# Kernel optimization log

Measured on AMD Instinct MI355X. Metric: run time of the kernel, lower is better.

Reference implementation:

```python
import jax, jax.numpy as jnp
import numpy as np

STRIDES = (8, 16, 32)
H = W = 640
SCORE_T = 0.5
NMS_T = 0.4


def setup_inputs() -> dict:
    key = jax.random.key(0)
    ks = jax.random.split(key, 9)
    feats = [(H // s) * (W // s) for s in STRIDES]  # 6400, 1600, 400
    d = {}
    for i, n in enumerate(feats):
        d[f"score{i}"] = jax.random.normal(ks[i], (1, n, 1), jnp.float32)
        d[f"bbox{i}"] = jax.random.normal(ks[3 + i], (1, n, 4), jnp.float32)
        d[f"kps{i}"] = jax.random.normal(ks[6 + i], (1, n, 10), jnp.float32)
    return d


def _anchors(stride):
    fh, fw = H // stride, W // stride
    yv, xv = jnp.meshgrid(jnp.arange(fh), jnp.arange(fw), indexing="ij")
    return jnp.stack([xv, yv], -1).reshape(-1, 2).astype(jnp.float32) * stride


def _decode(score, bbox, kps, stride):
    pts = _anchors(stride)                      # [N,2]
    s = jax.nn.sigmoid(score[0]).reshape(-1)    # [N]
    d = bbox[0] * stride                        # [N,4]
    x1 = pts[:, 0] - d[:, 0]
    y1 = pts[:, 1] - d[:, 1]
    x2 = pts[:, 0] + d[:, 2]
    y2 = pts[:, 1] + d[:, 3]
    b = jnp.stack([x1, y1, x2, y2], -1)         # [N,4]
    kd = (kps[0] * stride).reshape(-1, 5, 2)    # [N,5,2] (px,py pairs)
    k = (pts[:, None, :] + kd).reshape(-1, 10)  # [N,10]
    return s, b, k


def _iou(b):
    area = (b[:, 2] - b[:, 0]) * (b[:, 3] - b[:, 1])
    lt = jnp.maximum(b[:, None, :2], b[None, :, :2])
    rb = jnp.minimum(b[:, None, 2:], b[None, :, 2:])
    wh = jnp.clip(rb - lt, 0.0)
    inter = wh[..., 0] * wh[..., 1]
    return inter / (area[:, None] + area[None, :] - inter + 1e-9)


def _nms_keep(iou, valid, thresh):
    # greedy NMS on score-sorted boxes: keep i iff no earlier kept j has IoU>thresh
    n = valid.shape[0]
    def body(keep, xs):
        i, row = xs
        suppressed = jnp.any(keep & (row > thresh))
        keep = keep.at[i].set(valid[i] & ~suppressed)
        return keep, None
    keep, _ = jax.lax.scan(body, jnp.zeros(n, bool), (jnp.arange(n), iou))
    return keep


def reference(score0, score1, score2, bbox0, bbox1, bbox2, kps0, kps1, kps2):
    parts = [
        _decode(s, b, k, st)
        for s, b, k, st in zip(
            (score0, score1, score2), (bbox0, bbox1, bbox2), (kps0, kps1, kps2), STRIDES
        )
    ]
    scores = jnp.concatenate([p[0] for p in parts])  # [8400]
    boxes = jnp.concatenate([p[1] for p in parts])   # [8400,4]
    kpss = jnp.concatenate([p[2] for p in parts])    # [8400,10]
    order = jnp.argsort(-scores)                     # score-descending (NMS order)
    scores = scores[order]
    boxes = boxes[order]
    kpss = kpss[order]
    valid = scores > SCORE_T                         # threshold mask
    iou = _iou(jax.lax.stop_gradient(boxes))         # [8400,8400] ~282MB
    keep = _nms_keep(iou, valid, NMS_T)
    m = keep.astype(boxes.dtype)
    # fixed-shape equivalent of dynamic gather: suppressed rows zeroed, keep mask returned
    return boxes * m[:, None], scores * m, kpss * m[:, None], keep
```

## Files before the change

kernel.cpp:

```cpp
#include <hip/hip_runtime.h>
#include <math.h>

#define N_TOT 8400
#define MASK_WORDS 132
#define CAP 32
#define RT 33

typedef unsigned long long u64;

__device__ __forceinline__ unsigned mono_u32(float f) {
    unsigned u = __float_as_uint(f);
    return (u & 0x80000000u) ? ~u : (u | 0x80000000u);
}

__global__ void decode_kernel(const float* __restrict__ score0, const float* __restrict__ bbox0, const float* __restrict__ kps0,
                              const float* __restrict__ score1, const float* __restrict__ bbox1, const float* __restrict__ kps1,
                              const float* __restrict__ score2, const float* __restrict__ bbox2, const float* __restrict__ kps2,
                              float* __restrict__ logit, float* __restrict__ sig,
                              float* __restrict__ box, float* __restrict__ kps,
                              u64* __restrict__ key, int* __restrict__ rank,
                              unsigned int* __restrict__ cnt,
                              u64* __restrict__ validw, u64* __restrict__ rowflag) {
    int i = blockIdx.x * blockDim.x + threadIdx.x;
    if (i >= N_TOT) return;
    if (i < MASK_WORDS) { validw[i] = 0ull; rowflag[i] = 0ull; }
    rank[i] = 0;
    cnt[i] = 0u;
    const float *sc, *bb, *kp;
    int m, F; float s;
    if (i < 6400)      { sc = score0; bb = bbox0; kp = kps0; m = i;        F = 80; s = 8.f;  }
    else if (i < 8000) { sc = score1; bb = bbox1; kp = kps1; m = i - 6400; F = 40; s = 16.f; }
    else               { sc = score2; bb = bbox2; kp = kps2; m = i - 8000; F = 20; s = 32.f; }
    float px = (float)(m % F) * s;
    float py = (float)(m / F) * s;
    float lg = sc[m];
    logit[i] = lg;
    sig[i] = 1.0f / (1.0f + expf(-lg));
    key[i] = ((u64)(~mono_u32(lg)) << 14) | (u64)i;
    float d0 = bb[m*4+0]*s, d1 = bb[m*4+1]*s, d2 = bb[m*4+2]*s, d3 = bb[m*4+3]*s;
    box[i*4+0] = px - d0;
    box[i*4+1] = py - d1;
    box[i*4+2] = px + d2;
    box[i*4+3] = py + d3;
    #pragma unroll
    for (int c = 0; c < 5; ++c) {
        kps[i*10 + 2*c]   = px + kp[m*10 + 2*c]   * s;
        kps[i*10 + 2*c+1] = py + kp[m*10 + 2*c+1] * s;
    }
}

__global__ __launch_bounds__(256) void rank_kernel(const u64* __restrict__ key, int* __restrict__ rank) {
    __shared__ u64 tile[256];
    int i = blockIdx.x * 256 + threadIdx.x;
    int t0 = blockIdx.y * 256;
    u64 ki = (i < N_TOT) ? key[i] : 0ull;
    int j = t0 + threadIdx.x;
    tile[threadIdx.x] = (j < N_TOT) ? key[j] : ~0ull;
    __syncthreads();
    if (i >= N_TOT) return;
    int rk = 0;
    #pragma unroll 8
    for (int k = 0; k < 256; ++k) {
        rk += (tile[k] < ki) ? 1 : 0;
    }
    if (rk) atomicAdd(&rank[i], rk);
}

__global__ void scatter_kernel(const int* __restrict__ rank,
                               const float* __restrict__ logit, const float* __restrict__ sig,
                               const float* __restrict__ box, const float* __restrict__ kps,
                               float* __restrict__ s_logit, float* __restrict__ s_sig,
                               float* __restrict__ s_box, float* __restrict__ s_kps,
                               u64* __restrict__ validw) {
    int i = blockIdx.x * blockDim.x + threadIdx.x;
    if (i >= N_TOT) return;
    int r = rank[i];
    float lg = logit[i];
    s_logit[r] = lg;
    s_sig[r] = sig[i];
    #pragma unroll
    for (int c = 0; c < 4; ++c)  s_box[r*4+c] = box[i*4+c];
    #pragma unroll
    for (int c = 0; c < 10; ++c) s_kps[r*10+c] = kps[i*10+c];
    if (lg > 0.f) atomicOr(&validw[r >> 6], 1ull << (r & 63));
}

__global__ __launch_bounds__(64) void pairs_kernel(const float* __restrict__ s_logit,
                                                   const float* __restrict__ s_box,
                                                   unsigned int* __restrict__ cnt,
                                                   ulonglong2* __restrict__ ent,
                                                   u64* __restrict__ rowflag) {
    int cw = blockIdx.x;
    int rb = blockIdx.y;
    if (cw < rb) return;
    int tid = threadIdx.x;

    __shared__ float4 cbox[64];
    __shared__ float  carea[64];
    int j0 = cw * 64;
    int j = j0 + tid;
    float4 cb = make_float4(0.f, 0.f, 0.f, 0.f);
    float lgj = -1.f;
    if (j < N_TOT) {
        cb = ((const float4*)s_box)[j];
        lgj = s_logit[j];
    }
    cbox[tid] = cb;
    carea[tid] = (cb.z - cb.x) * (cb.w - cb.y);
    u64 cvalid = __ballot(j < N_TOT && lgj > 0.f);
    __syncthreads();
    if (cvalid == 0ull) return;

    int r = rb * 64 + tid;
    float lgr = (r < N_TOT) ? s_logit[r] : -1.f;
    if (__ballot(lgr > 0.f) == 0ull) return;

    u64 bits = 0ull;
    if (lgr > 0.f) {
        float4 rb4 = ((const float4*)s_box)[r];
        float rarea = (rb4.z - rb4.x) * (rb4.w - rb4.y);
        #pragma unroll 4
        for (int k = 0; k < 64; ++k) {
            float4 c4 = cbox[k];
            float ltx = fmaxf(rb4.x, c4.x);
            float lty = fmaxf(rb4.y, c4.y);
            float rbx = fminf(rb4.z, c4.z);
            float rby = fminf(rb4.w, c4.w);
            float w = fmaxf(rbx - ltx, 0.f);
            float h = fmaxf(rby - lty, 0.f);
            float inter = w * h;
            float iou = inter / (rarea + carea[k] - inter + 1e-9f);
            bits |= (iou > 0.4f) ? (1ull << k) : 0ull;
        }
        u64 m = cvalid;
        if (cw == rb) m &= (tid == 63) ? 0ull : (~0ull << (tid + 1));
        bits &= m;
    }
    if (bits) {
        unsigned idx = atomicAdd(&cnt[r], 1u);
        if (idx < CAP) {
            ulonglong2 e; e.x = bits; e.y = (u64)cw;
            ent[(size_t)r * CAP + idx] = e;
        }
        atomicOr(&rowflag[r >> 6], 1ull << (r & 63));
    }
}

__global__ __launch_bounds__(64) void nms_kernel(const u64* __restrict__ rowflag_g,
                                                 const u64* __restrict__ validw_g,
                                                 const unsigned int* __restrict__ cnt_g,
                                                 const ulonglong2* __restrict__ ent_g,
                                                 u64* __restrict__ keep_words) {
    __shared__ unsigned short list[8448];
    int lane = threadIdx.x;

    u64 rf[3], vw[3];
    #pragma unroll
    for (int s = 0; s < 3; ++s) {
        int w = s * 64 + lane;
        rf[s] = (w < MASK_WORDS) ? rowflag_g[w] : 0ull;
        vw[s] = (w < MASK_WORDS) ? validw_g[w] : 0ull;
    }

    int base = 0;
    #pragma unroll
    for (int s = 0; s < 3; ++s) {
        int c = (int)__popcll(rf[s]);
        int x = c;
        #pragma unroll
        for (int o = 1; o < 64; o <<= 1) { int y = __shfl_up(x, o); if (lane >= o) x += y; }
        int excl = x - c;
        int total = __shfl(x, 63);
        int off = base + excl;
        u64 t = rf[s];
        int wbase = (s * 64 + lane) << 6;
        while (t) {
            int b = __builtin_ctzll(t); t &= t - 1;
            list[off++] = (unsigned short)(wbase | b);
        }
        base += total;
    }
    int n_nz = base;
    __syncthreads();

    u64 rem0 = 0ull, rem1 = 0ull, rem2 = 0ull;

    if (n_nz > 0) {
        int half = lane >> 5;
        int sub  = lane & 31;

        int idx0 = min(sub, n_nz - 1);
        int rowCur = list[idx0];
        unsigned cntCur = cnt_g[rowCur];
        ulonglong2 entCur = ent_g[(size_t)rowCur * CAP + half];

        for (int k0 = 0; k0 < n_nz; k0 += 32) {
            int nb = k0 + 32;
            int rowNxt = 0; unsigned cntNxt = 0u;
            ulonglong2 entNxt; entNxt.x = 0ull; entNxt.y = 0ull;
            if (nb < n_nz) {
                int idx = min(nb + sub, n_nz - 1);
                rowNxt = list[idx];
                cntNxt = cnt_g[rowNxt];
                entNxt = ent_g[(size_t)rowNxt * CAP + half];
            }

            int lim = min(32, n_nz - k0);
            for (int i = 0; i < lim; ++i) {
                int r = __builtin_amdgcn_readlane(rowCur, i);
                int w = r >> 6, slot = w >> 6, owner = w & 63, b = r & 63;
                u64 rw = (slot == 0) ? rem0 : ((slot == 1) ? rem1 : rem2);
                unsigned halfw = (b < 32) ? (unsigned)rw : (unsigned)(rw >> 32);
                unsigned word = (unsigned)__builtin_amdgcn_readlane((int)halfw, owner);
                if (!((word >> (b & 31)) & 1u)) {
                    unsigned c = (unsigned)__builtin_amdgcn_readlane((int)cntCur, i);
                    int ec = (int)min(c, 2u);
                    for (int e = 0; e < ec; ++e) {
                        int src = e * 32 + i;
                        unsigned ey  = (unsigned)__builtin_amdgcn_readlane((int)(unsigned)entCur.y, src);
                        unsigned blo = (unsigned)__builtin_amdgcn_readlane((int)(unsigned)entCur.x, src);
                        unsigned bhi = (unsigned)__builtin_amdgcn_readlane((int)(unsigned)(entCur.x >> 32), src);
                        u64 bits = ((u64)bhi << 32) | (u64)blo;
                        int es = (int)(ey >> 6), eo = (int)(ey & 63u);
                        u64 add = (lane == eo) ? bits : 0ull;
                        if (es == 0) rem0 |= add; else if (es == 1) rem1 |= add; else rem2 |= add;
                    }
                    if (c > 2u) {
                        unsigned cm = min(c, (unsigned)CAP);
                        for (unsigned e = 2; e < cm; ++e) {
                            ulonglong2 g = ent_g[(size_t)r * CAP + e];
                            int es = (int)(g.y >> 6), eo = (int)(g.y & 63u);
                            u64 add = (lane == eo) ? g.x : 0ull;
                            if (es == 0) rem0 |= add; else if (es == 1) rem1 |= add; else rem2 |= add;
                        }
                    }
                }
            }
            rowCur = rowNxt; cntCur = cntNxt; entCur = entNxt;
        }
    }

    u64 rem[3] = {rem0, rem1, rem2};
    #pragma unroll
    for (int s = 0; s < 3; ++s) {
        int w = s * 64 + lane;
        if (w < MASK_WORDS) keep_words[w] = vw[s] & ~rem[s];
    }
}

__global__ void output_kernel(const float* __restrict__ s_sig, const float* __restrict__ s_box,
                              const float* __restrict__ s_kps,
                              const u64* __restrict__ keep_words,
                              float* __restrict__ out) {
    int r = blockIdx.x * blockDim.x + threadIdx.x;
    if (r >= N_TOT) return;
    float m = ((keep_words[r >> 6] >> (r & 63)) & 1ull) ? 1.0f : 0.0f;
    float* ob = out;
    float* os = out + 33600;
    float* okp = out + 42000;
    float* om = out + 126000;
    #pragma unroll
    for (int c = 0; c < 4; ++c)  ob[r*4+c] = s_box[r*4+c] * m;
    os[r] = s_sig[r] * m;
    #pragma unroll
    for (int c = 0; c < 10; ++c) okp[r*10+c] = s_kps[r*10+c] * m;
    om[r] = m;
}

extern "C" void kernel_launch(void* const* d_in, const int* in_sizes, int n_in,
                              void* d_out, int out_size, void* d_ws, size_t ws_size,
                              hipStream_t stream) {
    const float *score0, *bbox0, *kps0, *score1, *bbox1, *kps1, *score2, *bbox2, *kps2;
    if (in_sizes[1] == 25600) {
        score0 = (const float*)d_in[0]; bbox0 = (const float*)d_in[1]; kps0 = (const float*)d_in[2];
        score1 = (const float*)d_in[3]; bbox1 = (const float*)d_in[4]; kps1 = (const float*)d_in[5];
        score2 = (const float*)d_in[6]; bbox2 = (const float*)d_in[7]; kps2 = (const float*)d_in[8];
    } else {
        score0 = (const float*)d_in[0]; score1 = (const float*)d_in[1]; score2 = (const float*)d_in[2];
        bbox0  = (const float*)d_in[3]; bbox1  = (const float*)d_in[4]; bbox2  = (const float*)d_in[5];
        kps0   = (const float*)d_in[6]; kps1   = (const float*)d_in[7]; kps2   = (const float*)d_in[8];
    }

    char* ws = (char*)d_ws;
    float* logit   = (float*)(ws + 0);
    float* sig     = (float*)(ws + 33600);
    float* box     = (float*)(ws + 67200);
    float* kps     = (float*)(ws + 201600);
    int*   rank    = (int*)  (ws + 537600);
    float* s_logit = (float*)(ws + 571200);
    float* s_sig   = (float*)(ws + 604800);
    float* s_box   = (float*)(ws + 638400);
    float* s_kps   = (float*)(ws + 772800);
    u64*   keep_words = (u64*)(ws + 1108800);
    u64*   validw     = (u64*)(ws + 1110144);
    u64*   rowflag    = (u64*)(ws + 1111296);
    unsigned int* cnt = (unsigned int*)(ws + 1112448);
    u64*   key        = (u64*)(ws + 1146368);
    ulonglong2*   ent = (ulonglong2*)(ws + 1213568);

    float* out = (float*)d_out;

    decode_kernel<<<(N_TOT + 255) / 256, 256, 0, stream>>>(
        score0, bbox0, kps0, score1, bbox1, kps1, score2, bbox2, kps2,
        logit, sig, box, kps, key, rank, cnt, validw, rowflag);
    rank_kernel<<<dim3(RT, RT), 256, 0, stream>>>(key, rank);
    scatter_kernel<<<33, 256, 0, stream>>>(rank, logit, sig, box, kps,
                                           s_logit, s_sig, s_box, s_kps, validw);
    pairs_kernel<<<dim3(MASK_WORDS, MASK_WORDS), 64, 0, stream>>>(s_logit, s_box, cnt, ent, rowflag);
    nms_kernel<<<1, 64, 0, stream>>>(rowflag, validw, cnt, ent, keep_words);
    output_kernel<<<33, 256, 0, stream>>>(s_sig, s_box, s_kps, keep_words, out);
}
```

Before: 107.9 us.

## Restructure NMS scan to walk mask words with LDS removal bitmask

The single-wave NMS kernel no longer compacts a list of flagged rows. It now walks all 132 mask words in order, using valid&flagged bits per word, and keeps the removal mask in LDS updated with atomicOr. Within a word it suppresses intra-word bits through a per-row patch broadcast, and it prefetches the first two entries of the next word's 64 rows. This removes the prefix-scan compaction and the per-row readlane chain, at the cost of LDS atomics and serial per-bit ballots. The entry prefetch no longer hides global latency for sparse rows.

```diff
diff --git a/kernel.cpp b/kernel.cpp
--- a/kernel.cpp
+++ b/kernel.cpp
@@ -11,6 +11,12 @@
 __device__ __forceinline__ unsigned mono_u32(float f) {
     unsigned u = __float_as_uint(f);
     return (u & 0x80000000u) ? ~u : (u | 0x80000000u);
+}
+
+__device__ __forceinline__ u64 rl64(u64 v, int src) {
+    unsigned lo = (unsigned)__builtin_amdgcn_readlane((int)(unsigned)v, src);
+    unsigned hi = (unsigned)__builtin_amdgcn_readlane((int)(unsigned)(v >> 32), src);
+    return ((u64)hi << 32) | (u64)lo;
 }
 
 __global__ void decode_kernel(const float* __restrict__ score0, const float* __restrict__ bbox0, const float* __restrict__ kps0,
@@ -151,100 +157,97 @@
                                                  const unsigned int* __restrict__ cnt_g,
                                                  const ulonglong2* __restrict__ ent_g,
                                                  u64* __restrict__ keep_words) {
-    __shared__ unsigned short list[8448];
+    __shared__ unsigned remlo[MASK_WORDS];
+    __shared__ unsigned remhi[MASK_WORDS];
     int lane = threadIdx.x;
 
-    u64 rf[3], vw[3];
+    for (int w = lane; w < MASK_WORDS; w += 64) { remlo[w] = 0u; remhi[w] = 0u; }
+
+    u64 vwreg[3], efreg[3];
     #pragma unroll
     for (int s = 0; s < 3; ++s) {
         int w = s * 64 + lane;
-        rf[s] = (w < MASK_WORDS) ? rowflag_g[w] : 0ull;
-        vw[s] = (w < MASK_WORDS) ? validw_g[w] : 0ull;
-    }
-
-    int base = 0;
-    #pragma unroll
-    for (int s = 0; s < 3; ++s) {
-        int c = (int)__popcll(rf[s]);
-        int x = c;
-        #pragma unroll
-        for (int o = 1; o < 64; o <<= 1) { int y = __shfl_up(x, o); if (lane >= o) x += y; }
-        int excl = x - c;
-        int total = __shfl(x, 63);
-        int off = base + excl;
-        u64 t = rf[s];
-        int wbase = (s * 64 + lane) << 6;
-        while (t) {
-            int b = __builtin_ctzll(t); t &= t - 1;
-            list[off++] = (unsigned short)(wbase | b);
-        }
-        base += total;
-    }
-    int n_nz = base;
-    __syncthreads();
-
-    u64 rem0 = 0ull, rem1 = 0ull, rem2 = 0ull;
-
-    if (n_nz > 0) {
-        int half = lane >> 5;
-        int sub  = lane & 31;
-
-        int idx0 = min(sub, n_nz - 1);
-        int rowCur = list[idx0];
-        unsigned cntCur = cnt_g[rowCur];
-        ulonglong2 entCur = ent_g[(size_t)rowCur * CAP + half];
-
-        for (int k0 = 0; k0 < n_nz; k0 += 32) {
-            int nb = k0 + 32;
-            int rowNxt = 0; unsigned cntNxt = 0u;
-            ulonglong2 entNxt; entNxt.x = 0ull; entNxt.y = 0ull;
-            if (nb < n_nz) {
-                int idx = min(nb + sub, n_nz - 1);
-                rowNxt = list[idx];
-                cntNxt = cnt_g[rowNxt];
-                entNxt = ent_g[(size_t)rowNxt * CAP + half];
-            }
-
-            int lim = min(32, n_nz - k0);
-            for (int i = 0; i < lim; ++i) {
-                int r = __builtin_amdgcn_readlane(rowCur, i);
-                int w = r >> 6, slot = w >> 6, owner = w & 63, b = r & 63;
-                u64 rw = (slot == 0) ? rem0 : ((slot == 1) ? rem1 : rem2);
-                unsigned halfw = (b < 32) ? (unsigned)rw : (unsigned)(rw >> 32);
-                unsigned word = (unsigned)__builtin_amdgcn_readlane((int)halfw, owner);
-                if (!((word >> (b & 31)) & 1u)) {
-                    unsigned c = (unsigned)__builtin_amdgcn_readlane((int)cntCur, i);
-                    int ec = (int)min(c, 2u);
-                    for (int e = 0; e < ec; ++e) {
-                        int src = e * 32 + i;
-                        unsigned ey  = (unsigned)__builtin_amdgcn_readlane((int)(unsigned)entCur.y, src);
-                        unsigned blo = (unsigned)__builtin_amdgcn_readlane((int)(unsigned)entCur.x, src);
-                        unsigned bhi = (unsigned)__builtin_amdgcn_readlane((int)(unsigned)(entCur.x >> 32), src);
-                        u64 bits = ((u64)bhi << 32) | (u64)blo;
-                        int es = (int)(ey >> 6), eo = (int)(ey & 63u);
-                        u64 add = (lane == eo) ? bits : 0ull;
-                        if (es == 0) rem0 |= add; else if (es == 1) rem1 |= add; else rem2 |= add;
+        vwreg[s] = (w < MASK_WORDS) ? validw_g[w] : 0ull;
+        efreg[s] = (w < MASK_WORDS) ? rowflag_g[w] : 0ull;
+    }
+
+    unsigned cntC = cnt_g[lane];
+    ulonglong2 eAC = ent_g[(size_t)lane * CAP + 0];
+    ulonglong2 eBC = ent_g[(size_t)lane * CAP + 1];
+
+    for (int w = 0; w < MASK_WORDS; ++w) {
+        unsigned cntN = 0u;
+        ulonglong2 eAN; eAN.x = 0ull; eAN.y = 0ull;
+        ulonglong2 eBN; eBN.x = 0ull; eBN.y = 0ull;
+        int rn = (w + 1) * 64 + lane;
+        if (w + 1 < MASK_WORDS && rn < N_TOT) {
+            cntN = cnt_g[rn];
+            eAN = ent_g[(size_t)rn * CAP + 0];
+            eBN = ent_g[(size_t)rn * CAP + 1];
+        }
+
+        int slot = w >> 6, owner = w & 63;
+        u64 vw_s = rl64(vwreg[slot == 0 ? 0 : (slot == 1 ? 1 : 2)], owner);
+        u64 ef_s = rl64(efreg[slot == 0 ? 0 : (slot == 1 ? 1 : 2)], owner);
+        u64 b0 = vw_s & ef_s;
+        if (b0) {
+            unsigned rlo = remlo[w], rhi = remhi[w];
+            rlo = (unsigned)__builtin_amdgcn_readfirstlane((int)rlo);
+            rhi = (unsigned)__builtin_amdgcn_readfirstlane((int)rhi);
+            u64 remw = ((u64)rhi << 32) | (u64)rlo;
+            u64 beta = b0 & ~remw;
+            u64 totpatch = 0ull;
+            while (beta) {
+                int i = __builtin_ctzll(beta); beta &= beta - 1;
+                u64 patch = 0ull;
+                if (lane == i) {
+                    unsigned c = cntC;
+                    if (c > 0) {
+                        int tw = (int)eAC.y;
+                        if (tw == w) patch |= eAC.x;
+                        else { atomicOr(&remlo[tw], (unsigned)eAC.x); atomicOr(&remhi[tw], (unsigned)(eAC.x >> 32)); }
                     }
-                    if (c > 2u) {
+                    if (c > 1) {
+                        int tw = (int)eBC.y;
+                        if (tw == w) patch |= eBC.x;
+                        else { atomicOr(&remlo[tw], (unsigned)eBC.x); atomicOr(&remhi[tw], (unsigned)(eBC.x >> 32)); }
+                    }
+                    if (c > 2) {
                         unsigned cm = min(c, (unsigned)CAP);
+                        int r = w * 64 + i;
                         for (unsigned e = 2; e < cm; ++e) {
                             ulonglong2 g = ent_g[(size_t)r * CAP + e];
-                            int es = (int)(g.y >> 6), eo = (int)(g.y & 63u);
-                            u64 add = (lane == eo) ? g.x : 0ull;
-                            if (es == 0) rem0 |= add; else if (es == 1) rem1 |= add; else rem2 |= add;
+                            int tw = (int)g.y;
+                            if (tw == w) patch |= g.x;
+                            else { atomicOr(&remlo[tw], (unsigned)g.x); atomicOr(&remhi[tw], (unsigned)(g.x >> 32)); }
                         }
                     }
                 }
+                u64 pball = __ballot(patch != 0ull);
+                if (pball) {
+                    u64 pb = rl64(patch, i);
+                    beta &= ~pb;
+                    totpatch |= pb;
+                }
             }
-            rowCur = rowNxt; cntCur = cntNxt; entCur = entNxt;
-        }
-    }
-
-    u64 rem[3] = {rem0, rem1, rem2};
+            if (totpatch) {
+                if (lane == 0) {
+                    atomicOr(&remlo[w], (unsigned)totpatch);
+                    atomicOr(&remhi[w], (unsigned)(totpatch >> 32));
+                }
+            }
+        }
+        cntC = cntN; eAC = eAN; eBC = eBN;
+    }
+
+    __syncthreads();
     #pragma unroll
     for (int s = 0; s < 3; ++s) {
         int w = s * 64 + lane;
-        if (w < MASK_WORDS) keep_words[w] = vw[s] & ~rem[s];
+        if (w < MASK_WORDS) {
+            u64 rem = ((u64)remhi[w] << 32) | (u64)remlo[w];
+            keep_words[w] = vwreg[s] & ~rem;
+        }
     }
 }
 
```

Measured after the change: 168.3 us. 55.9% more time.

## Fuse all NMS stages into one cooperative persistent kernel with grid syncs

Applied to the files above, without the earlier changes.

Replaces six separate kernel launches (decode, rank, scatter, pairs, nms, output) with a single cooperative kernel of 256 blocks that separates the stages with grid.sync(). The pairs stage becomes a persistent triangular loop over upper-triangle tiles, with a closed-form index mapping, and reads column boxes through wave shuffles instead of shared memory. The aim is to remove the launch and inter-kernel gaps, which dominate at this small problem size. In exchange, the grid-wide barriers add cost, the serial NMS step runs in only one block while the rest of the grid waits, and the grid is capped at 256 blocks.

```diff
diff --git a/kernel.cpp b/kernel.cpp
--- a/kernel.cpp
+++ b/kernel.cpp
@@ -1,312 +1,307 @@
 #include <hip/hip_runtime.h>
+#include <hip/hip_cooperative_groups.h>
 #include <math.h>
+
+namespace cg = cooperative_groups;
 
 #define N_TOT 8400
 #define MASK_WORDS 132
 #define CAP 32
-#define RT 33
+#define GRID 256
+#define TPAIRS 8778
 
 typedef unsigned long long u64;
+
+struct MegaParams {
+    const float *score0, *bbox0, *kps0;
+    const float *score1, *bbox1, *kps1;
+    const float *score2, *bbox2, *kps2;
+    float *logit, *sig, *box, *kps;
+    float *s_logit, *s_sig, *s_box, *s_kps;
+    u64 *key;
+    int *rank;
+    unsigned int *cnt;
+    u64 *validw, *rowflag, *keep_words;
+    ulonglong2 *ent;
+    float *out;
+};
 
 __device__ __forceinline__ unsigned mono_u32(float f) {
     unsigned u = __float_as_uint(f);
     return (u & 0x80000000u) ? ~u : (u | 0x80000000u);
 }
 
-__global__ void decode_kernel(const float* __restrict__ score0, const float* __restrict__ bbox0, const float* __restrict__ kps0,
-                              const float* __restrict__ score1, const float* __restrict__ bbox1, const float* __restrict__ kps1,
-                              const float* __restrict__ score2, const float* __restrict__ bbox2, const float* __restrict__ kps2,
-                              float* __restrict__ logit, float* __restrict__ sig,
-                              float* __restrict__ box, float* __restrict__ kps,
-                              u64* __restrict__ key, int* __restrict__ rank,
-                              unsigned int* __restrict__ cnt,
-                              u64* __restrict__ validw, u64* __restrict__ rowflag) {
-    int i = blockIdx.x * blockDim.x + threadIdx.x;
-    if (i >= N_TOT) return;
-    if (i < MASK_WORDS) { validw[i] = 0ull; rowflag[i] = 0ull; }
-    rank[i] = 0;
-    cnt[i] = 0u;
-    const float *sc, *bb, *kp;
-    int m, F; float s;
-    if (i < 6400)      { sc = score0; bb = bbox0; kp = kps0; m = i;        F = 80; s = 8.f;  }
-    else if (i < 8000) { sc = score1; bb = bbox1; kp = kps1; m = i - 6400; F = 40; s = 16.f; }
-    else               { sc = score2; bb = bbox2; kp = kps2; m = i - 8000; F = 20; s = 32.f; }
-    float px = (float)(m % F) * s;
-    float py = (float)(m / F) * s;
-    float lg = sc[m];
-    logit[i] = lg;
-    sig[i] = 1.0f / (1.0f + expf(-lg));
-    key[i] = ((u64)(~mono_u32(lg)) << 14) | (u64)i;
-    float d0 = bb[m*4+0]*s, d1 = bb[m*4+1]*s, d2 = bb[m*4+2]*s, d3 = bb[m*4+3]*s;
-    box[i*4+0] = px - d0;
-    box[i*4+1] = py - d1;
-    box[i*4+2] = px + d2;
-    box[i*4+3] = py + d3;
-    #pragma unroll
-    for (int c = 0; c < 5; ++c) {
-        kps[i*10 + 2*c]   = px + kp[m*10 + 2*c]   * s;
-        kps[i*10 + 2*c+1] = py + kp[m*10 + 2*c+1] * s;
-    }
-}
-
-__global__ __launch_bounds__(256) void rank_kernel(const u64* __restrict__ key, int* __restrict__ rank) {
-    __shared__ u64 tile[256];
-    int i = blockIdx.x * 256 + threadIdx.x;
-    int t0 = blockIdx.y * 256;
-    u64 ki = (i < N_TOT) ? key[i] : 0ull;
-    int j = t0 + threadIdx.x;
-    tile[threadIdx.x] = (j < N_TOT) ? key[j] : ~0ull;
-    __syncthreads();
-    if (i >= N_TOT) return;
-    int rk = 0;
-    #pragma unroll 8
-    for (int k = 0; k < 256; ++k) {
-        rk += (tile[k] < ki) ? 1 : 0;
-    }
-    if (rk) atomicAdd(&rank[i], rk);
-}
-
-__global__ void scatter_kernel(const int* __restrict__ rank,
-                               const float* __restrict__ logit, const float* __restrict__ sig,
-                               const float* __restrict__ box, const float* __restrict__ kps,
-                               float* __restrict__ s_logit, float* __restrict__ s_sig,
-                               float* __restrict__ s_box, float* __restrict__ s_kps,
-                               u64* __restrict__ validw) {
-    int i = blockIdx.x * blockDim.x + threadIdx.x;
-    if (i >= N_TOT) return;
-    int r = rank[i];
-    float lg = logit[i];
-    s_logit[r] = lg;
-    s_sig[r] = sig[i];
-    #pragma unroll
-    for (int c = 0; c < 4; ++c)  s_box[r*4+c] = box[i*4+c];
-    #pragma unroll
-    for (int c = 0; c < 10; ++c) s_kps[r*10+c] = kps[i*10+c];
-    if (lg > 0.f) atomicOr(&validw[r >> 6], 1ull << (r & 63));
-}
-
-__global__ __launch_bounds__(64) void pairs_kernel(const float* __restrict__ s_logit,
-                                                   const float* __restrict__ s_box,
-                                                   unsigned int* __restrict__ cnt,
-                                                   ulonglong2* __restrict__ ent,
-                                                   u64* __restrict__ rowflag) {
-    int cw = blockIdx.x;
-    int rb = blockIdx.y;
-    if (cw < rb) return;
-    int tid = threadIdx.x;
-
-    __shared__ float4 cbox[64];
-    __shared__ float  carea[64];
-    int j0 = cw * 64;
-    int j = j0 + tid;
-    float4 cb = make_float4(0.f, 0.f, 0.f, 0.f);
-    float lgj = -1.f;
-    if (j < N_TOT) {
-        cb = ((const float4*)s_box)[j];
-        lgj = s_logit[j];
-    }
-    cbox[tid] = cb;
-    carea[tid] = (cb.z - cb.x) * (cb.w - cb.y);
-    u64 cvalid = __ballot(j < N_TOT && lgj > 0.f);
-    __syncthreads();
-    if (cvalid == 0ull) return;
-
-    int r = rb * 64 + tid;
-    float lgr = (r < N_TOT) ? s_logit[r] : -1.f;
-    if (__ballot(lgr > 0.f) == 0ull) return;
-
-    u64 bits = 0ull;
-    if (lgr > 0.f) {
-        float4 rb4 = ((const float4*)s_box)[r];
-        float rarea = (rb4.z - rb4.x) * (rb4.w - rb4.y);
-        #pragma unroll 4
-        for (int k = 0; k < 64; ++k) {
-            float4 c4 = cbox[k];
-            float ltx = fmaxf(rb4.x, c4.x);
-            float lty = fmaxf(rb4.y, c4.y);
-            float rbx = fminf(rb4.z, c4.z);
-            float rby = fminf(rb4.w, c4.w);
-            float w = fmaxf(rbx - ltx, 0.f);
-            float h = fmaxf(rby - lty, 0.f);
-            float inter = w * h;
-            float iou = inter / (rarea + carea[k] - inter + 1e-9f);
-            bits |= (iou > 0.4f) ? (1ull << k) : 0ull;
-        }
-        u64 m = cvalid;
-        if (cw == rb) m &= (tid == 63) ? 0ull : (~0ull << (tid + 1));
-        bits &= m;
-    }
-    if (bits) {
-        unsigned idx = atomicAdd(&cnt[r], 1u);
-        if (idx < CAP) {
-            ulonglong2 e; e.x = bits; e.y = (u64)cw;
-            ent[(size_t)r * CAP + idx] = e;
-        }
-        atomicOr(&rowflag[r >> 6], 1ull << (r & 63));
-    }
-}
-
-__global__ __launch_bounds__(64) void nms_kernel(const u64* __restrict__ rowflag_g,
-                                                 const u64* __restrict__ validw_g,
-                                                 const unsigned int* __restrict__ cnt_g,
-                                                 const ulonglong2* __restrict__ ent_g,
-                                                 u64* __restrict__ keep_words) {
-    __shared__ unsigned short list[8448];
-    int lane = threadIdx.x;
-
-    u64 rf[3], vw[3];
-    #pragma unroll
-    for (int s = 0; s < 3; ++s) {
-        int w = s * 64 + lane;
-        rf[s] = (w < MASK_WORDS) ? rowflag_g[w] : 0ull;
-        vw[s] = (w < MASK_WORDS) ? validw_g[w] : 0ull;
-    }
-
-    int base = 0;
-    #pragma unroll
-    for (int s = 0; s < 3; ++s) {
-        int c = (int)__popcll(rf[s]);
-        int x = c;
-        #pragma unroll
-        for (int o = 1; o < 64; o <<= 1) { int y = __shfl_up(x, o); if (lane >= o) x += y; }
-        int excl = x - c;
-        int total = __shfl(x, 63);
-        int off = base + excl;
-        u64 t = rf[s];
-        int wbase = (s * 64 + lane) << 6;
-        while (t) {
-            int b = __builtin_ctzll(t); t &= t - 1;
-            list[off++] = (unsigned short)(wbase | b);
-        }
-        base += total;
-    }
-    int n_nz = base;
-    __syncthreads();
-
-    u64 rem0 = 0ull, rem1 = 0ull, rem2 = 0ull;
-
-    if (n_nz > 0) {
-        int half = lane >> 5;
-        int sub  = lane & 31;
-
-        int idx0 = min(sub, n_nz - 1);
-        int rowCur = list[idx0];
-        unsigned cntCur = cnt_g[rowCur];
-        ulonglong2 entCur = ent_g[(size_t)rowCur * CAP + half];
-
-        for (int k0 = 0; k0 < n_nz; k0 += 32) {
-            int nb = k0 + 32;
-            int rowNxt = 0; unsigned cntNxt = 0u;
-            ulonglong2 entNxt; entNxt.x = 0ull; entNxt.y = 0ull;
-            if (nb < n_nz) {
-                int idx = min(nb + sub, n_nz - 1);
-                rowNxt = list[idx];
-                cntNxt = cnt_g[rowNxt];
-                entNxt = ent_g[(size_t)rowNxt * CAP + half];
-            }
-
-            int lim = min(32, n_nz - k0);
-            for (int i = 0; i < lim; ++i) {
-                int r = __builtin_amdgcn_readlane(rowCur, i);
-                int w = r >> 6, slot = w >> 6, owner = w & 63, b = r & 63;
-                u64 rw = (slot == 0) ? rem0 : ((slot == 1) ? rem1 : rem2);
-                unsigned halfw = (b < 32) ? (unsigned)rw : (unsigned)(rw >> 32);
-                unsigned word = (unsigned)__builtin_amdgcn_readlane((int)halfw, owner);
-                if (!((word >> (b & 31)) & 1u)) {
-                    unsigned c = (unsigned)__builtin_amdgcn_readlane((int)cntCur, i);
-                    int ec = (int)min(c, 2u);
-                    for (int e = 0; e < ec; ++e) {
-                        int src = e * 32 + i;
-                        unsigned ey  = (unsigned)__builtin_amdgcn_readlane((int)(unsigned)entCur.y, src);
-                        unsigned blo = (unsigned)__builtin_amdgcn_readlane((int)(unsigned)entCur.x, src);
-                        unsigned bhi = (unsigned)__builtin_amdgcn_readlane((int)(unsigned)(entCur.x >> 32), src);
-                        u64 bits = ((u64)bhi << 32) | (u64)blo;
-                        int es = (int)(ey >> 6), eo = (int)(ey & 63u);
-                        u64 add = (lane == eo) ? bits : 0ull;
-                        if (es == 0) rem0 |= add; else if (es == 1) rem1 |= add; else rem2 |= add;
+__global__ __launch_bounds__(256) void mega_kernel(MegaParams p) {
+    cg::grid_group grid = cg::this_grid();
+    const int tid  = threadIdx.x;
+    const int gtid = blockIdx.x * 256 + tid;
+
+    __shared__ u64 tileB[256];
+    __shared__ unsigned short nlist[8448];
+
+    if (gtid < N_TOT) {
+        int i = gtid;
+        if (i < MASK_WORDS) { p.validw[i] = 0ull; p.rowflag[i] = 0ull; }
+        p.rank[i] = 0;
+        p.cnt[i] = 0u;
+        const float *sc, *bb, *kp;
+        int m, F; float s;
+        if (i < 6400)      { sc = p.score0; bb = p.bbox0; kp = p.kps0; m = i;        F = 80; s = 8.f;  }
+        else if (i < 8000) { sc = p.score1; bb = p.bbox1; kp = p.kps1; m = i - 6400; F = 40; s = 16.f; }
+        else               { sc = p.score2; bb = p.bbox2; kp = p.kps2; m = i - 8000; F = 20; s = 32.f; }
+        float px = (float)(m % F) * s;
+        float py = (float)(m / F) * s;
+        float lg = sc[m];
+        p.logit[i] = lg;
+        p.sig[i] = 1.0f / (1.0f + expf(-lg));
+        p.key[i] = ((u64)(~mono_u32(lg)) << 14) | (u64)i;
+        float d0 = bb[m*4+0]*s, d1 = bb[m*4+1]*s, d2 = bb[m*4+2]*s, d3 = bb[m*4+3]*s;
+        p.box[i*4+0] = px - d0;
+        p.box[i*4+1] = py - d1;
+        p.box[i*4+2] = px + d2;
+        p.box[i*4+3] = py + d3;
+        #pragma unroll
+        for (int c = 0; c < 5; ++c) {
+            p.kps[i*10 + 2*c]   = px + kp[m*10 + 2*c]   * s;
+            p.kps[i*10 + 2*c+1] = py + kp[m*10 + 2*c+1] * s;
+        }
+    }
+    grid.sync();
+
+    for (int t = blockIdx.x; t < 33 * 33; t += GRID) {
+        int bi = t / 33, bj = t % 33;
+        int j = bj * 256 + tid;
+        tileB[tid] = (j < N_TOT) ? p.key[j] : ~0ull;
+        __syncthreads();
+        int i = bi * 256 + tid;
+        if (i < N_TOT) {
+            u64 ki = p.key[i];
+            int rk = 0;
+            #pragma unroll 8
+            for (int k = 0; k < 256; ++k) rk += (tileB[k] < ki) ? 1 : 0;
+            if (rk) atomicAdd(&p.rank[i], rk);
+        }
+        __syncthreads();
+    }
+    grid.sync();
+
+    if (gtid < N_TOT) {
+        int i = gtid;
+        int r = p.rank[i];
+        float lg = p.logit[i];
+        p.s_logit[r] = lg;
+        p.s_sig[r] = p.sig[i];
+        #pragma unroll
+        for (int c = 0; c < 4; ++c)  p.s_box[r*4+c] = p.box[i*4+c];
+        #pragma unroll
+        for (int c = 0; c < 10; ++c) p.s_kps[r*10+c] = p.kps[i*10+c];
+        if (lg > 0.f) atomicOr(&p.validw[r >> 6], 1ull << (r & 63));
+    }
+    grid.sync();
+
+    {
+        int wv = tid >> 6;
+        int lane = tid & 63;
+        int wgid = blockIdx.x * 4 + wv;
+        const float4* sbox4 = (const float4*)p.s_box;
+        for (int t = wgid; t < TPAIRS; t += GRID * 4) {
+            int rb = (int)((265.0 - sqrt(70225.0 - 8.0 * (double)t)) * 0.5);
+            while (rb > 0 && (rb * (265 - rb)) / 2 > t) --rb;
+            while (((rb + 1) * (265 - (rb + 1))) / 2 <= t) ++rb;
+            int cw = rb + (t - (rb * (265 - rb)) / 2);
+
+            int j = cw * 64 + lane;
+            float4 cb = make_float4(0.f, 0.f, 0.f, 0.f);
+            float lgj = -1.f;
+            if (j < N_TOT) { cb = sbox4[j]; lgj = p.s_logit[j]; }
+            u64 cvalid = __ballot(j < N_TOT && lgj > 0.f);
+            if (cvalid == 0ull) continue;
+
+            int r = rb * 64 + lane;
+            float lgr = (r < N_TOT) ? p.s_logit[r] : -1.f;
+            if (__ballot(lgr > 0.f) == 0ull) continue;
+
+            float4 rb4 = (r < N_TOT) ? sbox4[r] : make_float4(0.f, 0.f, 0.f, 0.f);
+            float rarea = (rb4.z - rb4.x) * (rb4.w - rb4.y);
+            float ca = (cb.z - cb.x) * (cb.w - cb.y);
+            u64 bits = 0ull;
+            #pragma unroll 4
+            for (int k = 0; k < 64; ++k) {
+                float cx1 = __shfl(cb.x, k);
+                float cy1 = __shfl(cb.y, k);
+                float cx2 = __shfl(cb.z, k);
+                float cy2 = __shfl(cb.w, k);
+                float cak = __shfl(ca, k);
+                float ltx = fmaxf(rb4.x, cx1);
+                float lty = fmaxf(rb4.y, cy1);
+                float rbx = fminf(rb4.z, cx2);
+                float rby = fminf(rb4.w, cy2);
+                float w = fmaxf(rbx - ltx, 0.f);
+                float h = fmaxf(rby - lty, 0.f);
+                float inter = w * h;
+                float iou = inter / (rarea + cak - inter + 1e-9f);
+                bits |= (iou > 0.4f) ? (1ull << k) : 0ull;
+            }
+            u64 m = cvalid;
+            if (cw == rb) m &= (lane == 63) ? 0ull : (~0ull << (lane + 1));
+            bits &= (lgr > 0.f) ? m : 0ull;
+
+            if (bits) {
+                unsigned idx = atomicAdd(&p.cnt[r], 1u);
+                if (idx < CAP) {
+                    ulonglong2 e; e.x = bits; e.y = (u64)cw;
+                    p.ent[(size_t)r * CAP + idx] = e;
+                }
+                atomicOr(&p.rowflag[r >> 6], 1ull << (r & 63));
+            }
+        }
+    }
+    grid.sync();
+
+    if (blockIdx.x == 0) {
+        int lane = tid;
+        u64 rf[3] = {0,0,0}, vw[3] = {0,0,0};
+        int n_nz = 0;
+        if (tid < 64) {
+            #pragma unroll
+            for (int s = 0; s < 3; ++s) {
+                int w = s * 64 + lane;
+                rf[s] = (w < MASK_WORDS) ? p.rowflag[w] : 0ull;
+                vw[s] = (w < MASK_WORDS) ? p.validw[w] : 0ull;
+            }
+            int base = 0;
+            #pragma unroll
+            for (int s = 0; s < 3; ++s) {
+                int c = (int)__popcll(rf[s]);
+                int x = c;
+                #pragma unroll
+                for (int o = 1; o < 64; o <<= 1) { int y = __shfl_up(x, o); if (lane >= o) x += y; }
+                int excl = x - c;
+                int total = __shfl(x, 63);
+                int off = base + excl;
+                u64 tt = rf[s];
+                int wbase = (s * 64 + lane) << 6;
+                while (tt) {
+                    int b = __builtin_ctzll(tt); tt &= tt - 1;
+                    nlist[off++] = (unsigned short)(wbase | b);
+                }
+                base += total;
+            }
+            n_nz = base;
+        }
+        __syncthreads();
+        if (tid < 64) {
+            u64 rem0 = 0ull, rem1 = 0ull, rem2 = 0ull;
+            if (n_nz > 0) {
+                int half = lane >> 5;
+                int sub  = lane & 31;
+                int idx0 = min(sub, n_nz - 1);
+                int rowCur = nlist[idx0];
+                unsigned cntCur = p.cnt[rowCur];
+                ulonglong2 entCur = p.ent[(size_t)rowCur * CAP + half];
+
+                for (int k0 = 0; k0 < n_nz; k0 += 32) {
+                    int nb = k0 + 32;
+                    int rowNxt = 0; unsigned cntNxt = 0u;
+                    ulonglong2 entNxt; entNxt.x = 0ull; entNxt.y = 0ull;
+                    if (nb < n_nz) {
+                        int idx = min(nb + sub, n_nz - 1);
+                        rowNxt = nlist[idx];
+                        cntNxt = p.cnt[rowNxt];
+                        entNxt = p.ent[(size_t)rowNxt * CAP + half];
                     }
-                    if (c > 2u) {
-                        unsigned cm = min(c, (unsigned)CAP);
-                        for (unsigned e = 2; e < cm; ++e) {
-                            ulonglong2 g = ent_g[(size_t)r * CAP + e];
-                            int es = (int)(g.y >> 6), eo = (int)(g.y & 63u);
-                            u64 add = (lane == eo) ? g.x : 0ull;
-                            if (es == 0) rem0 |= add; else if (es == 1) rem1 |= add; else rem2 |= add;
+                    int lim = min(32, n_nz - k0);
+                    for (int i = 0; i < lim; ++i) {
+                        int r = __builtin_amdgcn_readlane(rowCur, i);
+                        int w = r >> 6, slot = w >> 6, owner = w & 63, b = r & 63;
+                        u64 rw = (slot == 0) ? rem0 : ((slot == 1) ? rem1 : rem2);
+                        unsigned halfw = (b < 32) ? (unsigned)rw : (unsigned)(rw >> 32);
+                        unsigned word = (unsigned)__builtin_amdgcn_readlane((int)halfw, owner);
+                        if (!((word >> (b & 31)) & 1u)) {
+                            unsigned c = (unsigned)__builtin_amdgcn_readlane((int)cntCur, i);
+                            int ec = (int)min(c, 2u);
+                            for (int e = 0; e < ec; ++e) {
+                                int src = e * 32 + i;
+                                unsigned ey  = (unsigned)__builtin_amdgcn_readlane((int)(unsigned)entCur.y, src);
+                                unsigned blo = (unsigned)__builtin_amdgcn_readlane((int)(unsigned)entCur.x, src);
+                                unsigned bhi = (unsigned)__builtin_amdgcn_readlane((int)(unsigned)(entCur.x >> 32), src);
+                                u64 bits = ((u64)bhi << 32) | (u64)blo;
+                                int es = (int)(ey >> 6), eo = (int)(ey & 63u);
+                                u64 add = (lane == eo) ? bits : 0ull;
+                                if (es == 0) rem0 |= add; else if (es == 1) rem1 |= add; else rem2 |= add;
+                            }
+                            if (c > 2u) {
+                                unsigned cm = min(c, (unsigned)CAP);
+                                for (unsigned e = 2; e < cm; ++e) {
+                                    ulonglong2 g = p.ent[(size_t)r * CAP + e];
+                                    int es = (int)(g.y >> 6), eo = (int)(g.y & 63u);
+                                    u64 add = (lane == eo) ? g.x : 0ull;
+                                    if (es == 0) rem0 |= add; else if (es == 1) rem1 |= add; else rem2 |= add;
+                                }
+                            }
                         }
                     }
+                    rowCur = rowNxt; cntCur = cntNxt; entCur = entNxt;
                 }
             }
-            rowCur = rowNxt; cntCur = cntNxt; entCur = entNxt;
-        }
-    }
-
-    u64 rem[3] = {rem0, rem1, rem2};
-    #pragma unroll
-    for (int s = 0; s < 3; ++s) {
-        int w = s * 64 + lane;
-        if (w < MASK_WORDS) keep_words[w] = vw[s] & ~rem[s];
-    }
-}
-
-__global__ void output_kernel(const float* __restrict__ s_sig, const float* __restrict__ s_box,
-                              const float* __restrict__ s_kps,
-                              const u64* __restrict__ keep_words,
-                              float* __restrict__ out) {
-    int r = blockIdx.x * blockDim.x + threadIdx.x;
-    if (r >= N_TOT) return;
-    float m = ((keep_words[r >> 6] >> (r & 63)) & 1ull) ? 1.0f : 0.0f;
-    float* ob = out;
-    float* os = out + 33600;
-    float* okp = out + 42000;
-    float* om = out + 126000;
-    #pragma unroll
-    for (int c = 0; c < 4; ++c)  ob[r*4+c] = s_box[r*4+c] * m;
-    os[r] = s_sig[r] * m;
-    #pragma unroll
-    for (int c = 0; c < 10; ++c) okp[r*10+c] = s_kps[r*10+c] * m;
-    om[r] = m;
+            u64 rem[3] = {rem0, rem1, rem2};
+            #pragma unroll
+            for (int s = 0; s < 3; ++s) {
+                int w = s * 64 + lane;
+                if (w < MASK_WORDS) p.keep_words[w] = vw[s] & ~rem[s];
+            }
+        }
+    }
+    grid.sync();
+
+    if (gtid < N_TOT) {
+        int r = gtid;
+        float m = ((p.keep_words[r >> 6] >> (r & 63)) & 1ull) ? 1.0f : 0.0f;
+        float* ob = p.out;
+        float* os = p.out + 33600;
+        float* okp = p.out + 42000;
+        float* om = p.out + 126000;
+        #pragma unroll
+        for (int c = 0; c < 4; ++c)  ob[r*4+c] = p.s_box[r*4+c] * m;
+        os[r] = p.s_sig[r] * m;
+        #pragma unroll
+        for (int c = 0; c < 10; ++c) okp[r*10+c] = p.s_kps[r*10+c] * m;
+        om[r] = m;
+    }
 }
 
 extern "C" void kernel_launch(void* const* d_in, const int* in_sizes, int n_in,
                               void* d_out, int out_size, void* d_ws, size_t ws_size,
                               hipStream_t stream) {
-    const float *score0, *bbox0, *kps0, *score1, *bbox1, *kps1, *score2, *bbox2, *kps2;
+    MegaParams p;
     if (in_sizes[1] == 25600) {
-        score0 = (const float*)d_in[0]; bbox0 = (const float*)d_in[1]; kps0 = (const float*)d_in[2];
-        score1 = (const float*)d_in[3]; bbox1 = (const float*)d_in[4]; kps1 = (const float*)d_in[5];
-        score2 = (const float*)d_in[6]; bbox2 = (const float*)d_in[7]; kps2 = (const float*)d_in[8];
+        p.score0 = (const float*)d_in[0]; p.bbox0 = (const float*)d_in[1]; p.kps0 = (const float*)d_in[2];
+        p.score1 = (const float*)d_in[3]; p.bbox1 = (const float*)d_in[4]; p.kps1 = (const float*)d_in[5];
+        p.score2 = (const float*)d_in[6]; p.bbox2 = (const float*)d_in[7]; p.kps2 = (const float*)d_in[8];
     } else {
-        score0 = (const float*)d_in[0]; score1 = (const float*)d_in[1]; score2 = (const float*)d_in[2];
-        bbox0  = (const float*)d_in[3]; bbox1  = (const float*)d_in[4]; bbox2  = (const float*)d_in[5];
-        kps0   = (const float*)d_in[6]; kps1   = (const float*)d_in[7]; kps2   = (const float*)d_in[8];
+        p.score0 = (const float*)d_in[0]; p.score1 = (const float*)d_in[1]; p.score2 = (const float*)d_in[2];
+        p.bbox0  = (const float*)d_in[3]; p.bbox1  = (const float*)d_in[4]; p.bbox2  = (const float*)d_in[5];
+        p.kps0   = (const float*)d_in[6]; p.kps1   = (const float*)d_in[7]; p.kps2   = (const float*)d_in[8];
     }
 
     char* ws = (char*)d_ws;
-    float* logit   = (float*)(ws + 0);
-    float* sig     = (float*)(ws + 33600);
-    float* box     = (float*)(ws + 67200);
-    float* kps     = (float*)(ws + 201600);
-    int*   rank    = (int*)  (ws + 537600);
-    float* s_logit = (float*)(ws + 571200);
-    float* s_sig   = (float*)(ws + 604800);
-    float* s_box   = (float*)(ws + 638400);
-    float* s_kps   = (float*)(ws + 772800);
-    u64*   keep_words = (u64*)(ws + 1108800);
-    u64*   validw     = (u64*)(ws + 1110144);
-    u64*   rowflag    = (u64*)(ws + 1111296);
-    unsigned int* cnt = (unsigned int*)(ws + 1112448);
-    u64*   key        = (u64*)(ws + 1146368);
-    ulonglong2*   ent = (ulonglong2*)(ws + 1213568);
-
-    float* out = (float*)d_out;
-
-    decode_kernel<<<(N_TOT + 255) / 256, 256, 0, stream>>>(
-        score0, bbox0, kps0, score1, bbox1, kps1, score2, bbox2, kps2,
-        logit, sig, box, kps, key, rank, cnt, validw, rowflag);
-    rank_kernel<<<dim3(RT, RT), 256, 0, stream>>>(key, rank);
-    scatter_kernel<<<33, 256, 0, stream>>>(rank, logit, sig, box, kps,
-                                           s_logit, s_sig, s_box, s_kps, validw);
-    pairs_kernel<<<dim3(MASK_WORDS, MASK_WORDS), 64, 0, stream>>>(s_logit, s_box, cnt, ent, rowflag);
-    nms_kernel<<<1, 64, 0, stream>>>(rowflag, validw, cnt, ent, keep_words);
-    output_kernel<<<33, 256, 0, stream>>>(s_sig, s_box, s_kps, keep_words, out);
+    p.logit   = (float*)(ws + 0);
+    p.sig     = (float*)(ws + 33600);
+    p.box     = (float*)(ws + 67200);
+    p.kps     = (float*)(ws + 201600);
+    p.rank    = (int*)  (ws + 537600);
+    p.s_logit = (float*)(ws + 571200);
+    p.s_sig   = (float*)(ws + 604800);
+    p.s_box   = (float*)(ws + 638400);
+    p.s_kps   = (float*)(ws + 772800);
+    p.keep_words = (u64*)(ws + 1108800);
+    p.validw     = (u64*)(ws + 1110144);
+    p.rowflag    = (u64*)(ws + 1111296);
+    p.cnt = (unsigned int*)(ws + 1112448);
+    p.key = (u64*)(ws + 1146368);
+    p.ent = (ulonglong2*)(ws + 1213568);
+    p.out = (float*)d_out;
+
+    void* args[] = { &p };
+    hipLaunchCooperativeKernel((const void*)mega_kernel, dim3(GRID), dim3(256), args, 0, stream);
 }
```

Measured after the change: 273.9 us. 154% more time.
